# Performance work log

Hardware: AMD Instinct MI355X
Metric: run time of the kernel (lower is better)

## Reference

```python
import jax, jax.numpy as jnp
import numpy as np

POOL = 3      # pooling_size
EPS = 0.006   # constant added to each segment mean in the original code


def setup_inputs() -> dict:
    key = jax.random.key(0)
    k1, k2 = jax.random.split(key)
    B, N, D = 8, 3072, 1024          # N divisible by POOL -> no remainder branch
    steps = N // POOL
    x = jax.random.normal(k1, (B, N, D), dtype=jnp.float32)
    # (start, end) shot boundaries, sorted so start <= end, values in [0, N)
    graph = jnp.sort(jax.random.randint(k2, (B, steps, 2), 0, N, dtype=jnp.int64), axis=-1)
    return {"x": x, "graph": graph}


def reference(x, graph):
    B, N, D = x.shape
    steps = N // POOL
    # Exclusive+inclusive prefix sums: c[b, k] = sum over x[b, :k]  -> [B, N+1, D]
    c = jnp.concatenate([jnp.zeros((B, 1, D), x.dtype), jnp.cumsum(x, axis=1)], axis=1)
    s = graph[..., 0]                # [B, steps]
    e = graph[..., 1]                # [B, steps]
    idx_e = jnp.broadcast_to((e + 1)[..., None], (B, steps, D))
    idx_s = jnp.broadcast_to(s[..., None], (B, steps, D))
    seg_sum = jnp.take_along_axis(c, idx_e, axis=1) - jnp.take_along_axis(c, idx_s, axis=1)
    seg_len = (e - s + 1).astype(x.dtype)[..., None]
    seg_mean = seg_sum / seg_len + EPS            # [B, steps, D]
    # fixed-size window mean over consecutive POOL frames
    win_mean = x.reshape(B, steps, POOL, D).mean(axis=2)   # [B, steps, D]
    # original appends (segment mean, window mean) per step -> interleave
    out = jnp.stack([seg_mean, win_mean], axis=2).reshape(B, 2 * steps, D)
    return out
```

## Files before the change

kernel.cpp:

```cpp
#include <hip/hip_runtime.h>


constexpr int Bdim  = 8;
constexpr int Nn    = 3072;
constexpr int Dd    = 1024;
constexpr int STEPS = 1024;
constexpr int CHW   = 8;
constexpr int CHR   = 24;
constexpr int NCH   = 128;
constexpr int KT    = 4;
constexpr int NKT   = 256;
constexpr int D4    = Dd / 4;
constexpr int RCAP  = 16;
constexpr float EPS = 0.006f;

constexpr size_t T_E = (size_t)Bdim * 2 * STEPS * Dd;
constexpr size_t P_E = (size_t)Bdim * NCH * Dd;

typedef float nat_f4 __attribute__((ext_vector_type(4)));

__device__ __forceinline__ float4 f4add(float4 a, float4 b) {
    return make_float4(a.x + b.x, a.y + b.y, a.z + b.z, a.w + b.w);
}

__device__ __forceinline__ float4 f4sel(bool c, float4 a, float4 b) {
    return make_float4(c ? a.x : b.x, c ? a.y : b.y,
                       c ? a.z : b.z, c ? a.w : b.w);
}

__device__ __forceinline__ void nt_store(float4 v, float4* p) {
    nat_f4 nv = {v.x, v.y, v.z, v.w};
    __builtin_nontemporal_store(nv, reinterpret_cast<nat_f4*>(p));
}

__device__ __forceinline__ float4 nt_load(const float4* p) {
    nat_f4 nv = __builtin_nontemporal_load(reinterpret_cast<const nat_f4*>(p));
    return make_float4(nv.x, nv.y, nv.z, nv.w);
}

__global__ __launch_bounds__(256)
void k1_scan(const float4* __restrict__ x4, const int* __restrict__ graph,
             float4* __restrict__ out4, float4* __restrict__ T4,
             float4* __restrict__ P4) {
    const int t  = threadIdx.x;
    const int ch = blockIdx.x;
    const int b  = blockIdx.y;
    const int k0 = ch * CHW;
    const int r0 = ch * CHR;
    const float4 z4 = make_float4(0.f, 0.f, 0.f, 0.f);

    const float4* xp = x4 + ((size_t)(b * Nn + r0)) * D4 + t;
    float4 v[CHR];
#pragma unroll
    for (int i = 0; i < CHR; ++i)
        v[i] = nt_load(&xp[(size_t)i * D4]);

    __shared__ int cnt[CHR];
    __shared__ int lst[CHR][RCAP];
    if (t < CHR) cnt[t] = 0;
    __syncthreads();
    for (int k = t; k < STEPS; k += 256) {
        const int2 se = *reinterpret_cast<const int2*>(
            graph + ((size_t)(b * STEPS + k)) * 2);
        const int js = se.x - r0;
        if (js >= 0 && js < CHR) {
            int p = atomicAdd(&cnt[js], 1);
            if (p < RCAP) lst[js][p] = 2 * k;
        }
        const int je = se.y + 1 - r0;
        if (je >= 0 && je < CHR) {
            int p = atomicAdd(&cnt[je], 1);
            if (p < RCAP) lst[je][p] = 2 * k + 1;
        }
    }
    __syncthreads();

    float4* op = out4 + ((size_t)b * 2 * STEPS) * D4 + t;
#pragma unroll
    for (int wi = 0; wi < CHW; ++wi) {
        float4 w = f4add(f4add(v[3 * wi], v[3 * wi + 1]), v[3 * wi + 2]);
        float4 wm = make_float4(w.x * (1.f / 3.f), w.y * (1.f / 3.f),
                                w.z * (1.f / 3.f), w.w * (1.f / 3.f));
        nt_store(wm, &op[(size_t)(2 * (k0 + wi) + 1) * D4]);
    }

    float4* Tb = T4 + ((size_t)b * 2 * STEPS) * D4 + t;
    float4 run = z4;
#pragma unroll
    for (int j = 0; j < CHR; ++j) {
        const int nj = min(cnt[j], RCAP);
        for (int q = 0; q < nj; ++q)
            Tb[(size_t)lst[j][q] * D4] = run;
        run = f4add(run, v[j]);
    }
    P4[((size_t)b * NCH + ch) * D4 + t] = run;
}

__global__ __launch_bounds__(256)
void k2_chscan(const float4* __restrict__ P4, float4* __restrict__ O4) {
    __shared__ float4 part[8][33];
    const int cw  = threadIdx.x & 31;
    const int seg = threadIdx.x >> 5;
    const int col = blockIdx.x * 32 + cw;
    const int b   = blockIdx.y;

    const float4* p = P4 + (size_t)b * NCH * D4 + col;
    float4 v[16];
    float4 sum = make_float4(0.f, 0.f, 0.f, 0.f);
#pragma unroll
    for (int i = 0; i < 16; ++i) {
        v[i] = p[(size_t)(seg * 16 + i) * D4];
        sum = f4add(sum, v[i]);
    }
    part[seg][cw] = sum;
    __syncthreads();
    if (threadIdx.x < 32) {
        float4 run = make_float4(0.f, 0.f, 0.f, 0.f);
#pragma unroll
        for (int s = 0; s < 8; ++s) {
            float4 t2 = part[s][threadIdx.x];
            part[s][threadIdx.x] = run;
            run = f4add(run, t2);
        }
    }
    __syncthreads();
    float4 run = part[seg][cw];
    float4* o = O4 + (size_t)b * (NCH + 1) * D4 + col;
#pragma unroll
    for (int i = 0; i < 16; ++i) {
        o[(size_t)(seg * 16 + i) * D4] = run;
        run = f4add(run, v[i]);
    }
    if (seg == 7) o[(size_t)NCH * D4] = run;
}

__global__ __launch_bounds__(256)
void k4_combine(const float4* __restrict__ T4, const float4* __restrict__ O4,
                const int* __restrict__ graph, float4* __restrict__ out4) {
    const int t  = threadIdx.x;
    const int kt = blockIdx.x;
    const int b  = blockIdx.y;

    const int* gp = graph + ((size_t)(b * STEPS + kt * KT)) * 2;
    const int4 ga = *reinterpret_cast<const int4*>(gp);
    const int4 gb = *reinterpret_cast<const int4*>(gp + 4);
    const int sA[KT] = {ga.x, ga.z, gb.x, gb.z};
    const int eA[KT] = {ga.y, ga.w, gb.y, gb.w};

    const float4* Tb = T4 + (size_t)b * 2 * STEPS * D4 + t;
    const float4* oc = O4 + (size_t)b * (NCH + 1) * D4 + t;
    float4*       ob = out4 + (size_t)b * 2 * STEPS * D4 + t;

    float4 ts[KT], te[KT], o1[KT], o2[KT];
    int ieA[KT];
    const float4 tot = oc[(size_t)NCH * D4];
#pragma unroll
    for (int u = 0; u < KT; ++u) {
        const int k = kt * KT + u;
        ts[u] = Tb[(size_t)(2 * k) * D4];
        te[u] = Tb[(size_t)(2 * k + 1) * D4];
        const int s = sA[u];
        const int ie = eA[u] + 1;  ieA[u] = ie;
        o1[u] = oc[(size_t)(s / CHR) * D4];
        const int c2 = ie < Nn ? ie / CHR : 0;
        o2[u] = oc[(size_t)c2 * D4];
    }

#pragma unroll
    for (int u = 0; u < KT; ++u) {
        float4 cs = f4add(o1[u], ts[u]);
        float4 ce = f4sel(ieA[u] < Nn, f4add(o2[u], te[u]), tot);

        float inv = 1.f / (float)(eA[u] - sA[u] + 1);
        float4 res = make_float4((ce.x - cs.x) * inv + EPS,
                                 (ce.y - cs.y) * inv + EPS,
                                 (ce.z - cs.z) * inv + EPS,
                                 (ce.w - cs.w) * inv + EPS);
        const int k = kt * KT + u;
        nt_store(res, &ob[(size_t)(2 * k) * D4]);
    }
}

extern "C" void kernel_launch(void* const* d_in, const int* in_sizes, int n_in,
                              void* d_out, int out_size, void* d_ws, size_t ws_size,
                              hipStream_t stream) {
    const float* x     = (const float*)d_in[0];
    const int*   graph = (const int*)d_in[1];
    float*       out   = (float*)d_out;

    float* T = (float*)d_ws;
    float* P = T + T_E;
    float* O = P + P_E;

    dim3 g1(NCH, Bdim);
    k1_scan<<<g1, 256, 0, stream>>>((const float4*)x, graph, (float4*)out,
                                    (float4*)T, (float4*)P);
    dim3 g2(D4 / 32, Bdim);
    k2_chscan<<<g2, 256, 0, stream>>>((const float4*)P, (float4*)O);
    dim3 g4(NKT, Bdim);
    k4_combine<<<g4, 256, 0, stream>>>((const float4*)T, (const float4*)O,
                                       graph, (float4*)out);
}
```

Baseline: 182.3 us.

## Fold chunk-prefix scan into scan kernel via last-block-done atomic counter

Removes the separate chunk-scan kernel. Each scan block bumps a per-batch global counter after writing its partial sum, and the last block to finish for a batch serially scans all 128 chunk partials into the offset array. This saves one kernel launch and its dependency gap. In exchange it adds a memset launch and a serial 128-step scan done by a single block per batch on the critical path.

```diff
diff --git a/kernel.cpp b/kernel.cpp
--- a/kernel.cpp
+++ b/kernel.cpp
@@ -16,6 +16,7 @@
 
 constexpr size_t T_E = (size_t)Bdim * 2 * STEPS * Dd;
 constexpr size_t P_E = (size_t)Bdim * NCH * Dd;
+constexpr size_t O_E = (size_t)Bdim * (NCH + 1) * Dd;
 
 typedef float nat_f4 __attribute__((ext_vector_type(4)));
 
@@ -41,7 +42,8 @@
 __global__ __launch_bounds__(256)
 void k1_scan(const float4* __restrict__ x4, const int* __restrict__ graph,
              float4* __restrict__ out4, float4* __restrict__ T4,
-             float4* __restrict__ P4) {
+             float4* __restrict__ P4, float4* __restrict__ O4,
+             int* __restrict__ cnt) {
     const int t  = threadIdx.x;
     const int ch = blockIdx.x;
     const int b  = blockIdx.y;
@@ -55,21 +57,21 @@
     for (int i = 0; i < CHR; ++i)
         v[i] = nt_load(&xp[(size_t)i * D4]);
 
-    __shared__ int cnt[CHR];
+    __shared__ int scnt[CHR];
     __shared__ int lst[CHR][RCAP];
-    if (t < CHR) cnt[t] = 0;
+    if (t < CHR) scnt[t] = 0;
     __syncthreads();
     for (int k = t; k < STEPS; k += 256) {
         const int2 se = *reinterpret_cast<const int2*>(
             graph + ((size_t)(b * STEPS + k)) * 2);
         const int js = se.x - r0;
         if (js >= 0 && js < CHR) {
-            int p = atomicAdd(&cnt[js], 1);
+            int p = atomicAdd(&scnt[js], 1);
             if (p < RCAP) lst[js][p] = 2 * k;
         }
         const int je = se.y + 1 - r0;
         if (je >= 0 && je < CHR) {
-            int p = atomicAdd(&cnt[je], 1);
+            int p = atomicAdd(&scnt[je], 1);
             if (p < RCAP) lst[je][p] = 2 * k + 1;
         }
     }
@@ -88,50 +90,38 @@
     float4 run = z4;
 #pragma unroll
     for (int j = 0; j < CHR; ++j) {
-        const int nj = min(cnt[j], RCAP);
+        const int nj = min(scnt[j], RCAP);
         for (int q = 0; q < nj; ++q)
             Tb[(size_t)lst[j][q] * D4] = run;
         run = f4add(run, v[j]);
     }
     P4[((size_t)b * NCH + ch) * D4 + t] = run;
-}
 
-__global__ __launch_bounds__(256)
-void k2_chscan(const float4* __restrict__ P4, float4* __restrict__ O4) {
-    __shared__ float4 part[8][33];
-    const int cw  = threadIdx.x & 31;
-    const int seg = threadIdx.x >> 5;
-    const int col = blockIdx.x * 32 + cw;
-    const int b   = blockIdx.y;
-
-    const float4* p = P4 + (size_t)b * NCH * D4 + col;
-    float4 v[16];
-    float4 sum = make_float4(0.f, 0.f, 0.f, 0.f);
-#pragma unroll
-    for (int i = 0; i < 16; ++i) {
-        v[i] = p[(size_t)(seg * 16 + i) * D4];
-        sum = f4add(sum, v[i]);
-    }
-    part[seg][cw] = sum;
+    __threadfence();
     __syncthreads();
-    if (threadIdx.x < 32) {
-        float4 run = make_float4(0.f, 0.f, 0.f, 0.f);
-#pragma unroll
-        for (int s = 0; s < 8; ++s) {
-            float4 t2 = part[s][threadIdx.x];
-            part[s][threadIdx.x] = run;
-            run = f4add(run, t2);
-        }
+    __shared__ int s_last;
+    if (t == 0) {
+        int old = __hip_atomic_fetch_add(&cnt[b], 1, __ATOMIC_ACQ_REL,
+                                         __HIP_MEMORY_SCOPE_AGENT);
+        s_last = (old == NCH - 1);
     }
     __syncthreads();
-    float4 run = part[seg][cw];
-    float4* o = O4 + (size_t)b * (NCH + 1) * D4 + col;
-#pragma unroll
-    for (int i = 0; i < 16; ++i) {
-        o[(size_t)(seg * 16 + i) * D4] = run;
-        run = f4add(run, v[i]);
+    if (s_last) {
+        const float4* pb = P4 + (size_t)b * NCH * D4 + t;
+        float4*       o  = O4 + (size_t)b * (NCH + 1) * D4 + t;
+        float4 run2 = z4;
+        for (int c = 0; c < NCH; c += 4) {
+            float4 p0 = pb[(size_t)(c + 0) * D4];
+            float4 p1 = pb[(size_t)(c + 1) * D4];
+            float4 p2 = pb[(size_t)(c + 2) * D4];
+            float4 p3 = pb[(size_t)(c + 3) * D4];
+            o[(size_t)(c + 0) * D4] = run2;  run2 = f4add(run2, p0);
+            o[(size_t)(c + 1) * D4] = run2;  run2 = f4add(run2, p1);
+            o[(size_t)(c + 2) * D4] = run2;  run2 = f4add(run2, p2);
+            o[(size_t)(c + 3) * D4] = run2;  run2 = f4add(run2, p3);
+        }
+        o[(size_t)NCH * D4] = run2;
     }
-    if (seg == 7) o[(size_t)NCH * D4] = run;
 }
 
 __global__ __launch_bounds__(256)
@@ -191,12 +181,13 @@
     float* T = (float*)d_ws;
     float* P = T + T_E;
     float* O = P + P_E;
+    int*   cnt = (int*)(O + O_E);
+
+    hipMemsetAsync(cnt, 0, Bdim * sizeof(int), stream);
 
     dim3 g1(NCH, Bdim);
     k1_scan<<<g1, 256, 0, stream>>>((const float4*)x, graph, (float4*)out,
-                                    (float4*)T, (float4*)P);
-    dim3 g2(D4 / 32, Bdim);
-    k2_chscan<<<g2, 256, 0, stream>>>((const float4*)P, (float4*)O);
+                                    (float4*)T, (float4*)P, (float4*)O, cnt);
     dim3 g4(NKT, Bdim);
     k4_combine<<<g4, 256, 0, stream>>>((const float4*)T, (const float4*)O,
                                        graph, (float4*)out);
```

Result: slower. 393.4 us (+115.8%).
